# Kernel tuning notes

Hardware: AMD Instinct MI355X
Metric: run time of the kernel (lower is better)

The kernel has to match this reference:

```python
import math
import jax, jax.numpy as jnp
import numpy as np

B, S, D, H = 2, 2048, 1024, 16
HD = D // H  # head_dim = 64
LN_EPS = 1e-5


def setup_inputs() -> dict:
    key = jax.random.key(0)
    ks = jax.random.split(key, 12)
    scale = 1.0 / math.sqrt(D)
    inp = {
        "x": jax.random.normal(ks[0], (B, S, D), dtype=jnp.float32),
        "cdr_mask": jax.random.uniform(ks[1], (B, 1, S, S), dtype=jnp.float32),
        "Wq": jax.random.normal(ks[2], (D, D), dtype=jnp.float32) * scale,
        "bq": jnp.zeros((D,), dtype=jnp.float32),
        "Wk": jax.random.normal(ks[3], (D, D), dtype=jnp.float32) * scale,
        "bk": jnp.zeros((D,), dtype=jnp.float32),
        "Wv": jax.random.normal(ks[4], (D, D), dtype=jnp.float32) * scale,
        "bv": jnp.zeros((D,), dtype=jnp.float32),
        "Wo": jax.random.normal(ks[5], (D, D), dtype=jnp.float32) * scale,
        "bo": jnp.zeros((D,), dtype=jnp.float32),
        "gamma": jnp.ones((D,), dtype=jnp.float32),
        "beta": jnp.zeros((D,), dtype=jnp.float32),
        "cdr_weight": jnp.float32(1.0),
    }
    return inp


def _rotate_half(t):
    # even / odd interleaved halves, as in the torch module
    t1 = t[..., ::2]
    t2 = t[..., 1::2]
    return jnp.stack((-t2, t1), axis=-1).reshape(t.shape)


def reference(x, cdr_mask, Wq, bq, Wk, bk, Wv, bv, Wo, bo, gamma, beta, cdr_weight):
    b, s, d = x.shape
    # RoPE tables (concatenated, NOT interleaved -- faithful to source)
    inv_freq = 1.0 / (10000.0 ** (jnp.arange(0, HD, 2, dtype=jnp.float32) / HD))
    pos = jnp.arange(s, dtype=jnp.float32)
    sinusoid = pos[:, None] * inv_freq[None, :]          # [S, HD/2]
    sin_pos = jnp.concatenate([jnp.sin(sinusoid)] * 2, axis=-1)[None, None]  # [1,1,S,HD]
    cos_pos = jnp.concatenate([jnp.cos(sinusoid)] * 2, axis=-1)[None, None]

    def proj(W, bias):
        return (x @ W.T + bias).reshape(b, s, H, HD).transpose(0, 2, 1, 3)  # [B,H,S,HD]

    Q = proj(Wq, bq)
    K = proj(Wk, bk)
    V = proj(Wv, bv)
    Q = Q * cos_pos + _rotate_half(Q) * sin_pos
    K = K * cos_pos + _rotate_half(K) * sin_pos

    scores = jnp.einsum('bhqd,bhkd->bhqk', Q, K) / math.sqrt(HD)
    scores = scores + cdr_mask * cdr_weight
    probs = jax.nn.softmax(scores, axis=-1)
    attn = jnp.einsum('bhqk,bhkd->bhqd', probs, V)       # [B,H,S,HD]
    attn = attn.transpose(0, 2, 1, 3).reshape(b, s, d)
    out = attn @ Wo.T + bo                               # dropout is identity at eval

    y = x + out
    mu = jnp.mean(y, axis=-1, keepdims=True)
    var = jnp.var(y, axis=-1, keepdims=True)
    return (y - mu) / jnp.sqrt(var + LN_EPS) * gamma + beta
```

## Files before the change

kernel.cpp:

```cpp
#include <hip/hip_runtime.h>
#include <hip/hip_bf16.h>
#include <math.h>

#define Bn  2
#define Sn  2048
#define Dn  1024
#define Hn  16
#define HDn 64

typedef __attribute__((ext_vector_type(8))) short bf16x8;
typedef __attribute__((ext_vector_type(4))) short bf16x4;
typedef __attribute__((ext_vector_type(4))) float f32x4;

__device__ __forceinline__ uint2 pack4bf(float a, float b, float c, float d) {
    union { __hip_bfloat16 h[4]; uint2 u; } p;
    p.h[0] = __float2bfloat16(a); p.h[1] = __float2bfloat16(b);
    p.h[2] = __float2bfloat16(c); p.h[3] = __float2bfloat16(d);
    return p.u;
}

__device__ __forceinline__ bf16x4 pack4bfv(float a, float b, float c, float d) {
    union { __hip_bfloat16 h[4]; bf16x4 v; } p;
    p.h[0] = __float2bfloat16(a); p.h[1] = __float2bfloat16(b);
    p.h[2] = __float2bfloat16(c); p.h[3] = __float2bfloat16(d);
    return p.v;
}

__device__ __forceinline__ void g2l16(const __hip_bfloat16* g, __hip_bfloat16* lbase) {
    __builtin_amdgcn_global_load_lds(
        (const __attribute__((address_space(1))) void*)g,
        (__attribute__((address_space(3))) void*)lbase, 16, 0, 0);
}

__global__ __launch_bounds__(256) void cast_kernel(
    const float* __restrict__ in, __hip_bfloat16* __restrict__ out)
{
    const size_t i = ((size_t)blockIdx.x * 256 + threadIdx.x) * 4;
    float4 v = *(const float4*)(in + i);
    *(uint2*)(out + i) = pack4bf(v.x, v.y, v.z, v.w);
}

__global__ __launch_bounds__(256) void maskprep_kernel(
    const float* __restrict__ mask, const float* __restrict__ cwp,
    __hip_bfloat16* __restrict__ Mw)
{
    const int idx = blockIdx.x * 256 + threadIdx.x;
    const float cw = cwp[0];
    float4 v = ((const float4*)mask)[idx];
    ((uint2*)Mw)[idx] = pack4bf(v.x * cw, v.y * cw, v.z * cw, v.w * cw);
}

template<int MODE>
__global__ __launch_bounds__(256) void projmm(
    const __hip_bfloat16* __restrict__ X,
    const __hip_bfloat16* __restrict__ Wb,
    const float* __restrict__ bias,
    const float* __restrict__ resid,
    void* __restrict__ outp)
{
    __shared__ __hip_bfloat16 Xs[128 * 32];
    __shared__ __hip_bfloat16 Ws[64 * 32];
    const int tid  = threadIdx.x;
    const int w    = tid >> 6, lane = tid & 63;
    const int lrow = lane & 15, lhi = lane >> 4;
    const int m0   = blockIdx.y * 128, n0 = blockIdx.x * 64;
    const int rin  = lane >> 2, cbs = lane & 3;

    f32x4 acc[8];
#pragma unroll
    for (int i = 0; i < 8; i++) acc[i] = (f32x4){0.f, 0.f, 0.f, 0.f};

    for (int k0 = 0; k0 < Dn; k0 += 32) {
        const int xr0 = w * 32 + rin;
        const int xr1 = xr0 + 16;
        const int wr  = w * 16 + rin;
        g2l16(X  + (size_t)(m0 + xr0) * Dn + k0 + ((cbs ^ ((xr0 >> 1) & 3)) << 3),
              &Xs[(w * 32) * 32]);
        g2l16(X  + (size_t)(m0 + xr1) * Dn + k0 + ((cbs ^ ((xr1 >> 1) & 3)) << 3),
              &Xs[(w * 32 + 16) * 32]);
        g2l16(Wb + (size_t)(n0 + wr) * Dn + k0 + ((cbs ^ ((wr >> 1) & 3)) << 3),
              &Ws[(w * 16) * 32]);
        __syncthreads();

        bf16x8 FX[2], FW[4];
#pragma unroll
        for (int tm = 0; tm < 2; tm++) {
            const int r = w * 32 + tm * 16 + lrow;
            FX[tm] = *(const bf16x8*)&Xs[r * 32 + ((lhi ^ ((r >> 1) & 3)) << 3)];
        }
#pragma unroll
        for (int tn = 0; tn < 4; tn++) {
            const int r = tn * 16 + lrow;
            FW[tn] = *(const bf16x8*)&Ws[r * 32 + ((lhi ^ ((r >> 1) & 3)) << 3)];
        }
        if constexpr (MODE == 3) {
#pragma unroll
            for (int tm = 0; tm < 2; tm++)
#pragma unroll
                for (int tn = 0; tn < 4; tn++)
                    acc[tm * 4 + tn] = __builtin_amdgcn_mfma_f32_16x16x32_bf16(
                        FX[tm], FW[tn], acc[tm * 4 + tn], 0, 0, 0);
        } else {
#pragma unroll
            for (int tn = 0; tn < 4; tn++)
#pragma unroll
                for (int tm = 0; tm < 2; tm++)
                    acc[tn * 2 + tm] = __builtin_amdgcn_mfma_f32_16x16x32_bf16(
                        FW[tn], FX[tm], acc[tn * 2 + tm], 0, 0, 0);
        }
        __syncthreads();
    }

    const int h = n0 >> 6;

    if constexpr (MODE == 1 || MODE == 4) {
        __hip_bfloat16* outb = (__hip_bfloat16*)outp;
        const float NEG_L2C = -0.41524101186092033f;
#pragma unroll
        for (int tn = 0; tn < 4; tn++) {
            const int hd0 = tn * 16 + lhi * 4;
            const float4 b4 = *(const float4*)&bias[n0 + hd0];
            const float f0 = exp2f((float)((hd0 + 0) & 31) * NEG_L2C);
            const float f1 = exp2f((float)((hd0 + 1) & 31) * NEG_L2C);
            const float f2 = exp2f((float)((hd0 + 2) & 31) * NEG_L2C);
            const float f3 = exp2f((float)((hd0 + 3) & 31) * NEG_L2C);
#pragma unroll
            for (int tm = 0; tm < 2; tm++) {
                const int m = m0 + w * 32 + tm * 16 + lrow;
                const int s = m & (Sn - 1), bb = m >> 11;
                f32x4 a = acc[tn * 2 + tm];
                float v0 = a[0] + b4.x, v1 = a[1] + b4.y;
                float v2 = a[2] + b4.z, v3 = a[3] + b4.w;
                if (MODE == 1) { v0 *= 0.125f; v1 *= 0.125f; v2 *= 0.125f; v3 *= 0.125f; }
                const float sf = (float)s;
                const float c0 = __cosf(sf * f0), c1 = __cosf(sf * f1);
                const float c2 = __cosf(sf * f2), c3 = __cosf(sf * f3);
                const float s0 = __sinf(sf * f0), s1 = __sinf(sf * f1);
                const float s2 = __sinf(sf * f2), s3 = __sinf(sf * f3);
                const float r0 = v0 * c0 - v1 * s0;
                const float r1 = v1 * c1 + v0 * s1;
                const float r2 = v2 * c2 - v3 * s2;
                const float r3 = v3 * c3 + v2 * s3;
                *(uint2*)(outb + ((size_t)(bb * Hn + h) * Sn + s) * HDn + hd0) =
                    pack4bf(r0, r1, r2, r3);
            }
        }
    } else if constexpr (MODE == 3) {
        __hip_bfloat16* outb = (__hip_bfloat16*)outp;
#pragma unroll
        for (int tn = 0; tn < 4; tn++) {
            const int c = tn * 16 + lrow;
            const float bc = bias[n0 + c];
#pragma unroll
            for (int tm = 0; tm < 2; tm++) {
                const int mb = m0 + w * 32 + tm * 16 + lhi * 4;
                const int s = mb & (Sn - 1), bb = mb >> 11;
                f32x4 a = acc[tm * 4 + tn];
                *(uint2*)(outb + ((size_t)(bb * Hn + h) * HDn + c) * Sn + s) =
                    pack4bf(a[0] + bc, a[1] + bc, a[2] + bc, a[3] + bc);
            }
        }
    } else {
        float* outf = (float*)outp;
#pragma unroll
        for (int tn = 0; tn < 4; tn++) {
            const int nb = n0 + tn * 16 + lhi * 4;
            const float4 b4 = *(const float4*)&bias[nb];
#pragma unroll
            for (int tm = 0; tm < 2; tm++) {
                const int m = m0 + w * 32 + tm * 16 + lrow;
                f32x4 a = acc[tn * 2 + tm];
                const float4 rr = *(const float4*)&resid[(size_t)m * Dn + nb];
                *(float4*)(outf + (size_t)m * Dn + nb) =
                    make_float4(a[0] + b4.x + rr.x, a[1] + b4.y + rr.y,
                                a[2] + b4.z + rr.z, a[3] + b4.w + rr.w);
            }
        }
    }
}

struct __align__(16) TileBuf {
    __hip_bfloat16 K[64 * 64];
    __hip_bfloat16 V[64 * 64];
    __hip_bfloat16 M[64 * 64];
};

__device__ __forceinline__ void stage_tiles(
    TileBuf& t,
    const __hip_bfloat16* __restrict__ Kb,
    const __hip_bfloat16* __restrict__ Vb,
    const __hip_bfloat16* __restrict__ Mq0,
    int k0, int w, int lane)
{
#pragma unroll
    for (int j = 0; j < 2; j++) {
        const int row = w * 16 + j * 8 + (lane >> 3);
        const int blk = (lane & 7) ^ (row & 7);
        __hip_bfloat16* base = (__hip_bfloat16*)0;
        base = &((TileBuf&)t).K[(w * 16 + j * 8) * 64];
        g2l16(Kb + (size_t)(k0 + row) * HDn + blk * 8, base);
        base = &((TileBuf&)t).V[(w * 16 + j * 8) * 64];
        g2l16(Vb + (size_t)row * Sn + k0 + blk * 8, base);
        base = &((TileBuf&)t).M[(w * 16 + j * 8) * 64];
        g2l16(Mq0 + (size_t)row * Sn + k0 + blk * 8, base);
    }
}

__global__ __launch_bounds__(256) void attn_kernel(
    const __hip_bfloat16* __restrict__ Q,
    const __hip_bfloat16* __restrict__ K,
    const __hip_bfloat16* __restrict__ Vt,
    const __hip_bfloat16* __restrict__ Mw,
    __hip_bfloat16* __restrict__ A)
{
    __shared__ TileBuf tb[2];
    const int tid  = threadIdx.x;
    const int w    = tid >> 6, lane = tid & 63;
    const int lrow = lane & 15, lhi = lane >> 4;
    const int bh   = blockIdx.y, b = bh >> 4, h = bh & 15;
    const int q0   = blockIdx.x * 64;
    const int q    = q0 + w * 16 + lrow;

    const __hip_bfloat16* Qp  = Q + ((size_t)bh * Sn + q) * HDn + lhi * 8;
    const bf16x8 Qf0 = *(const bf16x8*)(Qp);
    const bf16x8 Qf1 = *(const bf16x8*)(Qp + 32);
    const __hip_bfloat16* Kb  = K  + (size_t)bh * Sn * HDn;
    const __hip_bfloat16* Vb  = Vt + (size_t)bh * HDn * Sn;
    const __hip_bfloat16* Mq0 = Mw + ((size_t)b * Sn + q0) * Sn;

    f32x4 Oc[4];
#pragma unroll
    for (int i = 0; i < 4; i++) Oc[i] = (f32x4){0.f, 0.f, 0.f, 0.f};
    float lsum = 0.f;

    stage_tiles(tb[0], Kb, Vb, Mq0, 0, w, lane);
    __syncthreads();

    for (int it = 0; it < Sn / 64; it++) {
        const int k0 = it * 64;
        if (it + 1 < Sn / 64)
            stage_tiles(tb[(it + 1) & 1], Kb, Vb, Mq0, k0 + 64, w, lane);
        const TileBuf& t = tb[it & 1];

        f32x4 st[4];
#pragma unroll
        for (int kt = 0; kt < 4; kt++) {
            const int rl = kt * 16 + lrow;
            const bf16x8 ka = *(const bf16x8*)&t.K[rl * 64 + ((lhi       ^ (rl & 7)) * 8)];
            const bf16x8 kc = *(const bf16x8*)&t.K[rl * 64 + (((4 + lhi) ^ (rl & 7)) * 8)];
            f32x4 z = (f32x4){0.f, 0.f, 0.f, 0.f};
            z = __builtin_amdgcn_mfma_f32_16x16x32_bf16(ka, Qf0, z, 0, 0, 0);
            z = __builtin_amdgcn_mfma_f32_16x16x32_bf16(kc, Qf1, z, 0, 0, 0);
            st[kt] = z;
        }

        const int rq = w * 16 + lrow;
        bf16x4 pk[4];
#pragma unroll
        for (int kt = 0; kt < 4; kt++) {
            const int eo = (((2 * kt + (lhi >> 1)) ^ (rq & 7)) * 8) + (lhi & 1) * 4;
            union { uint2 u; __hip_bfloat16 hh[4]; } mu;
            mu.u = *(const uint2*)&t.M[rq * 64 + eo];
            const float p0 = __expf(st[kt][0] + __bfloat162float(mu.hh[0]));
            const float p1 = __expf(st[kt][1] + __bfloat162float(mu.hh[1]));
            const float p2 = __expf(st[kt][2] + __bfloat162float(mu.hh[2]));
            const float p3 = __expf(st[kt][3] + __bfloat162float(mu.hh[3]));
            lsum += (p0 + p1) + (p2 + p3);
            pk[kt] = pack4bfv(p0, p1, p2, p3);
        }

#pragma unroll
        for (int ch = 0; ch < 4; ch++) {
            const int rv = ch * 16 + lrow;
#pragma unroll
            for (int kt = 0; kt < 4; kt++) {
                const int eo = (((2 * kt + (lhi >> 1)) ^ (rv & 7)) * 8) + (lhi & 1) * 4;
                const bf16x4 vf = *(const bf16x4*)&t.V[rv * 64 + eo];
                Oc[ch] = __builtin_amdgcn_mfma_f32_16x16x16bf16_1k(
                    vf, pk[kt], Oc[ch], 0, 0, 0);
            }
        }
        __syncthreads();
    }

    lsum += __shfl_xor(lsum, 16, 64);
    lsum += __shfl_xor(lsum, 32, 64);
    const float inv = 1.f / lsum;

    __hip_bfloat16* ap = A + ((size_t)(b * Sn + q)) * Dn + h * HDn;
#pragma unroll
    for (int ch = 0; ch < 4; ch++) {
        *(uint2*)(ap + ch * 16 + lhi * 4) =
            pack4bf(Oc[ch][0] * inv, Oc[ch][1] * inv, Oc[ch][2] * inv, Oc[ch][3] * inv);
    }
}

__global__ __launch_bounds__(256) void ln_kernel(
    const float* __restrict__ Yin, const float* __restrict__ gamma,
    const float* __restrict__ beta, float* __restrict__ out)
{
    __shared__ float red[256];
    const int m   = blockIdx.x;
    const int tid = threadIdx.x;
    const size_t base = (size_t)m * Dn + tid * 4;
    float4 y = *(const float4*)(Yin + base);

    red[tid] = y.x + y.y + y.z + y.w; __syncthreads();
    for (int off = 128; off > 0; off >>= 1) {
        if (tid < off) red[tid] += red[tid + off];
        __syncthreads();
    }
    const float mu = red[0] * (1.f / Dn);
    __syncthreads();

    const float d0 = y.x - mu, d1 = y.y - mu, d2 = y.z - mu, d3 = y.w - mu;
    red[tid] = d0*d0 + d1*d1 + d2*d2 + d3*d3; __syncthreads();
    for (int off = 128; off > 0; off >>= 1) {
        if (tid < off) red[tid] += red[tid + off];
        __syncthreads();
    }
    const float var = red[0] * (1.f / Dn);
    const float rin = rsqrtf(var + 1e-5f);

    float4 gv = *(const float4*)(gamma + tid * 4);
    float4 bv = *(const float4*)(beta  + tid * 4);
    *(float4*)(out + base) = make_float4(d0 * rin * gv.x + bv.x,
                                         d1 * rin * gv.y + bv.y,
                                         d2 * rin * gv.z + bv.z,
                                         d3 * rin * gv.w + bv.w);
}

extern "C" void kernel_launch(void* const* d_in, const int* in_sizes, int n_in,
                              void* d_out, int out_size, void* d_ws, size_t ws_size,
                              hipStream_t stream)
{
    const float* x     = (const float*)d_in[0];
    const float* mask  = (const float*)d_in[1];
    const float* Wq    = (const float*)d_in[2];
    const float* bq    = (const float*)d_in[3];
    const float* Wk    = (const float*)d_in[4];
    const float* bk    = (const float*)d_in[5];
    const float* Wv    = (const float*)d_in[6];
    const float* bv    = (const float*)d_in[7];
    const float* Wo    = (const float*)d_in[8];
    const float* bo    = (const float*)d_in[9];
    const float* gamma = (const float*)d_in[10];
    const float* beta  = (const float*)d_in[11];
    const float* cw    = (const float*)d_in[12];
    float* out = (float*)d_out;

    const size_t MB = 1024 * 1024;
    char* ws = (char*)d_ws;
    __hip_bfloat16* Xb  = (__hip_bfloat16*)(ws);
    __hip_bfloat16* Qb  = (__hip_bfloat16*)(ws +  8 * MB);
    __hip_bfloat16* Kb  = (__hip_bfloat16*)(ws + 16 * MB);
    __hip_bfloat16* Vtb = (__hip_bfloat16*)(ws + 24 * MB);
    __hip_bfloat16* Mw  = (__hip_bfloat16*)(ws + 32 * MB);
    __hip_bfloat16* Wqb = (__hip_bfloat16*)(ws + 48 * MB);
    __hip_bfloat16* Wkb = (__hip_bfloat16*)(ws + 50 * MB);
    __hip_bfloat16* Wvb = (__hip_bfloat16*)(ws + 52 * MB);
    __hip_bfloat16* Wob = (__hip_bfloat16*)(ws + 54 * MB);
    __hip_bfloat16* Ab  = Xb;

    cast_kernel<<<4096, 256, 0, stream>>>(x,  Xb);
    cast_kernel<<<1024, 256, 0, stream>>>(Wq, Wqb);
    cast_kernel<<<1024, 256, 0, stream>>>(Wk, Wkb);
    cast_kernel<<<1024, 256, 0, stream>>>(Wv, Wvb);
    cast_kernel<<<1024, 256, 0, stream>>>(Wo, Wob);
    maskprep_kernel<<<(Bn * Sn * Sn / 4) / 256, 256, 0, stream>>>(mask, cw, Mw);

    dim3 g(Dn / 64, (Bn * Sn) / 128);
    projmm<1><<<g, 256, 0, stream>>>(Xb, Wqb, bq, nullptr, Qb);
    projmm<4><<<g, 256, 0, stream>>>(Xb, Wkb, bk, nullptr, Kb);
    projmm<3><<<g, 256, 0, stream>>>(Xb, Wvb, bv, nullptr, Vtb);
    attn_kernel<<<dim3(Sn / 64, Bn * Hn), 256, 0, stream>>>(Qb, Kb, Vtb, Mw, Ab);
    projmm<2><<<g, 256, 0, stream>>>(Ab, Wob, bo, x, out);
    ln_kernel<<<Bn * Sn, 256, 0, stream>>>(out, gamma, beta, out);
}
```

Baseline: 304.2 us.

## Enlarge projection GEMM tiles, use exp2 softmax, warp-shuffle LayerNorm, paired bf16 packing

Projection GEMMs move from 128x64 to 128x128 block tiles with a 2x2 wave layout, so each wave computes a 64x64 subtile and more work is reused per LDS load. The grid halves, which may reduce occupancy. The softmax pre-scales Q and the mask by log2(e) so attention can use the hardware exp2 instead of __expf. LayerNorm replaces the shared-memory tree reductions with wave shuffles and a single-pass sum and sum-of-squares, which is slightly less numerically stable. bf16 packing now uses paired conversions.

```diff
diff --git a/kernel.cpp b/kernel.cpp
--- a/kernel.cpp
+++ b/kernel.cpp
@@ -12,17 +12,23 @@
 typedef __attribute__((ext_vector_type(4))) short bf16x4;
 typedef __attribute__((ext_vector_type(4))) float f32x4;
 
+#define LOG2E 1.44269504088896340736f
+
+__device__ __forceinline__ float fexp2(float x) {
+    return __builtin_amdgcn_exp2f(x);
+}
+
 __device__ __forceinline__ uint2 pack4bf(float a, float b, float c, float d) {
-    union { __hip_bfloat16 h[4]; uint2 u; } p;
-    p.h[0] = __float2bfloat16(a); p.h[1] = __float2bfloat16(b);
-    p.h[2] = __float2bfloat16(c); p.h[3] = __float2bfloat16(d);
+    union { __hip_bfloat162 h2[2]; uint2 u; } p;
+    p.h2[0] = __float22bfloat162_rn(make_float2(a, b));
+    p.h2[1] = __float22bfloat162_rn(make_float2(c, d));
     return p.u;
 }
 
 __device__ __forceinline__ bf16x4 pack4bfv(float a, float b, float c, float d) {
-    union { __hip_bfloat16 h[4]; bf16x4 v; } p;
-    p.h[0] = __float2bfloat16(a); p.h[1] = __float2bfloat16(b);
-    p.h[2] = __float2bfloat16(c); p.h[3] = __float2bfloat16(d);
+    union { __hip_bfloat162 h2[2]; bf16x4 v; } p;
+    p.h2[0] = __float22bfloat162_rn(make_float2(a, b));
+    p.h2[1] = __float22bfloat162_rn(make_float2(c, d));
     return p.v;
 }
 
@@ -45,7 +51,7 @@
     __hip_bfloat16* __restrict__ Mw)
 {
     const int idx = blockIdx.x * 256 + threadIdx.x;
-    const float cw = cwp[0];
+    const float cw = cwp[0] * LOG2E;
     float4 v = ((const float4*)mask)[idx];
     ((uint2*)Mw)[idx] = pack4bf(v.x * cw, v.y * cw, v.z * cw, v.w * cw);
 }
@@ -59,43 +65,40 @@
     void* __restrict__ outp)
 {
     __shared__ __hip_bfloat16 Xs[128 * 32];
-    __shared__ __hip_bfloat16 Ws[64 * 32];
+    __shared__ __hip_bfloat16 Ws[128 * 32];
     const int tid  = threadIdx.x;
     const int w    = tid >> 6, lane = tid & 63;
     const int lrow = lane & 15, lhi = lane >> 4;
-    const int m0   = blockIdx.y * 128, n0 = blockIdx.x * 64;
-    const int rin  = lane >> 2, cbs = lane & 3;
-
-    f32x4 acc[8];
-#pragma unroll
-    for (int i = 0; i < 8; i++) acc[i] = (f32x4){0.f, 0.f, 0.f, 0.f};
+    const int m0   = blockIdx.y * 128, n0 = blockIdx.x * 128;
+    const int rm   = (w & 1) * 64;
+    const int rn   = (w >> 1) * 64;
+    const int srow = lane >> 2, cb = lane & 3;
+
+    f32x4 acc[16];
+#pragma unroll
+    for (int i = 0; i < 16; i++) acc[i] = (f32x4){0.f, 0.f, 0.f, 0.f};
 
     for (int k0 = 0; k0 < Dn; k0 += 32) {
-        const int xr0 = w * 32 + rin;
-        const int xr1 = xr0 + 16;
-        const int wr  = w * 16 + rin;
-        g2l16(X  + (size_t)(m0 + xr0) * Dn + k0 + ((cbs ^ ((xr0 >> 1) & 3)) << 3),
-              &Xs[(w * 32) * 32]);
-        g2l16(X  + (size_t)(m0 + xr1) * Dn + k0 + ((cbs ^ ((xr1 >> 1) & 3)) << 3),
-              &Xs[(w * 32 + 16) * 32]);
-        g2l16(Wb + (size_t)(n0 + wr) * Dn + k0 + ((cbs ^ ((wr >> 1) & 3)) << 3),
-              &Ws[(w * 16) * 32]);
+#pragma unroll
+        for (int j = 0; j < 2; j++) {
+            const int row = w * 32 + j * 16 + srow;
+            const int sc  = (cb ^ ((row >> 1) & 3)) << 3;
+            g2l16(X  + (size_t)(m0 + row) * Dn + k0 + sc, &Xs[(w * 32 + j * 16) * 32]);
+            g2l16(Wb + (size_t)(n0 + row) * Dn + k0 + sc, &Ws[(w * 32 + j * 16) * 32]);
+        }
         __syncthreads();
 
-        bf16x8 FX[2], FW[4];
-#pragma unroll
-        for (int tm = 0; tm < 2; tm++) {
-            const int r = w * 32 + tm * 16 + lrow;
-            FX[tm] = *(const bf16x8*)&Xs[r * 32 + ((lhi ^ ((r >> 1) & 3)) << 3)];
-        }
-#pragma unroll
-        for (int tn = 0; tn < 4; tn++) {
-            const int r = tn * 16 + lrow;
-            FW[tn] = *(const bf16x8*)&Ws[r * 32 + ((lhi ^ ((r >> 1) & 3)) << 3)];
+        bf16x8 FX[4], FW[4];
+#pragma unroll
+        for (int t = 0; t < 4; t++) {
+            const int ra = rm + t * 16 + lrow;
+            FX[t] = *(const bf16x8*)&Xs[ra * 32 + ((lhi ^ ((ra >> 1) & 3)) << 3)];
+            const int rb = rn + t * 16 + lrow;
+            FW[t] = *(const bf16x8*)&Ws[rb * 32 + ((lhi ^ ((rb >> 1) & 3)) << 3)];
         }
         if constexpr (MODE == 3) {
 #pragma unroll
-            for (int tm = 0; tm < 2; tm++)
+            for (int tm = 0; tm < 4; tm++)
 #pragma unroll
                 for (int tn = 0; tn < 4; tn++)
                     acc[tm * 4 + tn] = __builtin_amdgcn_mfma_f32_16x16x32_bf16(
@@ -104,34 +107,34 @@
 #pragma unroll
             for (int tn = 0; tn < 4; tn++)
 #pragma unroll
-                for (int tm = 0; tm < 2; tm++)
-                    acc[tn * 2 + tm] = __builtin_amdgcn_mfma_f32_16x16x32_bf16(
-                        FW[tn], FX[tm], acc[tn * 2 + tm], 0, 0, 0);
+                for (int tm = 0; tm < 4; tm++)
+                    acc[tn * 4 + tm] = __builtin_amdgcn_mfma_f32_16x16x32_bf16(
+                        FW[tn], FX[tm], acc[tn * 4 + tm], 0, 0, 0);
         }
         __syncthreads();
     }
-
-    const int h = n0 >> 6;
 
     if constexpr (MODE == 1 || MODE == 4) {
         __hip_bfloat16* outb = (__hip_bfloat16*)outp;
+        const int h = (n0 >> 6) + (w >> 1);
         const float NEG_L2C = -0.41524101186092033f;
+        const float SCL = 0.125f * LOG2E;
 #pragma unroll
         for (int tn = 0; tn < 4; tn++) {
             const int hd0 = tn * 16 + lhi * 4;
-            const float4 b4 = *(const float4*)&bias[n0 + hd0];
+            const float4 b4 = *(const float4*)&bias[n0 + rn + hd0];
             const float f0 = exp2f((float)((hd0 + 0) & 31) * NEG_L2C);
             const float f1 = exp2f((float)((hd0 + 1) & 31) * NEG_L2C);
             const float f2 = exp2f((float)((hd0 + 2) & 31) * NEG_L2C);
             const float f3 = exp2f((float)((hd0 + 3) & 31) * NEG_L2C);
 #pragma unroll
-            for (int tm = 0; tm < 2; tm++) {
-                const int m = m0 + w * 32 + tm * 16 + lrow;
+            for (int tm = 0; tm < 4; tm++) {
+                const int m = m0 + rm + tm * 16 + lrow;
                 const int s = m & (Sn - 1), bb = m >> 11;
-                f32x4 a = acc[tn * 2 + tm];
+                f32x4 a = acc[tn * 4 + tm];
                 float v0 = a[0] + b4.x, v1 = a[1] + b4.y;
                 float v2 = a[2] + b4.z, v3 = a[3] + b4.w;
-                if (MODE == 1) { v0 *= 0.125f; v1 *= 0.125f; v2 *= 0.125f; v3 *= 0.125f; }
+                if (MODE == 1) { v0 *= SCL; v1 *= SCL; v2 *= SCL; v3 *= SCL; }
                 const float sf = (float)s;
                 const float c0 = __cosf(sf * f0), c1 = __cosf(sf * f1);
                 const float c2 = __cosf(sf * f2), c3 = __cosf(sf * f3);
@@ -147,13 +150,14 @@
         }
     } else if constexpr (MODE == 3) {
         __hip_bfloat16* outb = (__hip_bfloat16*)outp;
+        const int h = (n0 >> 6) + (w >> 1);
 #pragma unroll
         for (int tn = 0; tn < 4; tn++) {
             const int c = tn * 16 + lrow;
-            const float bc = bias[n0 + c];
-#pragma unroll
-            for (int tm = 0; tm < 2; tm++) {
-                const int mb = m0 + w * 32 + tm * 16 + lhi * 4;
+            const float bc = bias[n0 + rn + c];
+#pragma unroll
+            for (int tm = 0; tm < 4; tm++) {
+                const int mb = m0 + rm + tm * 16 + lhi * 4;
                 const int s = mb & (Sn - 1), bb = mb >> 11;
                 f32x4 a = acc[tm * 4 + tn];
                 *(uint2*)(outb + ((size_t)(bb * Hn + h) * HDn + c) * Sn + s) =
@@ -164,12 +168,12 @@
         float* outf = (float*)outp;
 #pragma unroll
         for (int tn = 0; tn < 4; tn++) {
-            const int nb = n0 + tn * 16 + lhi * 4;
+            const int nb = n0 + rn + tn * 16 + lhi * 4;
             const float4 b4 = *(const float4*)&bias[nb];
 #pragma unroll
-            for (int tm = 0; tm < 2; tm++) {
-                const int m = m0 + w * 32 + tm * 16 + lrow;
-                f32x4 a = acc[tn * 2 + tm];
+            for (int tm = 0; tm < 4; tm++) {
+                const int m = m0 + rm + tm * 16 + lrow;
+                f32x4 a = acc[tn * 4 + tm];
                 const float4 rr = *(const float4*)&resid[(size_t)m * Dn + nb];
                 *(float4*)(outf + (size_t)m * Dn + nb) =
                     make_float4(a[0] + b4.x + rr.x, a[1] + b4.y + rr.y,
@@ -196,13 +200,9 @@
     for (int j = 0; j < 2; j++) {
         const int row = w * 16 + j * 8 + (lane >> 3);
         const int blk = (lane & 7) ^ (row & 7);
-        __hip_bfloat16* base = (__hip_bfloat16*)0;
-        base = &((TileBuf&)t).K[(w * 16 + j * 8) * 64];
-        g2l16(Kb + (size_t)(k0 + row) * HDn + blk * 8, base);
-        base = &((TileBuf&)t).V[(w * 16 + j * 8) * 64];
-        g2l16(Vb + (size_t)row * Sn + k0 + blk * 8, base);
-        base = &((TileBuf&)t).M[(w * 16 + j * 8) * 64];
-        g2l16(Mq0 + (size_t)row * Sn + k0 + blk * 8, base);
+        g2l16(Kb + (size_t)(k0 + row) * HDn + blk * 8, &t.K[(w * 16 + j * 8) * 64]);
+        g2l16(Vb + (size_t)row * Sn + k0 + blk * 8,    &t.V[(w * 16 + j * 8) * 64]);
+        g2l16(Mq0 + (size_t)row * Sn + k0 + blk * 8,   &t.M[(w * 16 + j * 8) * 64]);
     }
 }
 
@@ -261,10 +261,10 @@
             const int eo = (((2 * kt + (lhi >> 1)) ^ (rq & 7)) * 8) + (lhi & 1) * 4;
             union { uint2 u; __hip_bfloat16 hh[4]; } mu;
             mu.u = *(const uint2*)&t.M[rq * 64 + eo];
-            const float p0 = __expf(st[kt][0] + __bfloat162float(mu.hh[0]));
-            const float p1 = __expf(st[kt][1] + __bfloat162float(mu.hh[1]));
-            const float p2 = __expf(st[kt][2] + __bfloat162float(mu.hh[2]));
-            const float p3 = __expf(st[kt][3] + __bfloat162float(mu.hh[3]));
+            const float p0 = fexp2(st[kt][0] + __bfloat162float(mu.hh[0]));
+            const float p1 = fexp2(st[kt][1] + __bfloat162float(mu.hh[1]));
+            const float p2 = fexp2(st[kt][2] + __bfloat162float(mu.hh[2]));
+            const float p3 = fexp2(st[kt][3] + __bfloat162float(mu.hh[3]));
             lsum += (p0 + p1) + (p2 + p3);
             pk[kt] = pack4bfv(p0, p1, p2, p3);
         }
@@ -299,35 +299,33 @@
     const float* __restrict__ Yin, const float* __restrict__ gamma,
     const float* __restrict__ beta, float* __restrict__ out)
 {
-    __shared__ float red[256];
+    __shared__ float2 wred[4];
     const int m   = blockIdx.x;
     const int tid = threadIdx.x;
     const size_t base = (size_t)m * Dn + tid * 4;
     float4 y = *(const float4*)(Yin + base);
 
-    red[tid] = y.x + y.y + y.z + y.w; __syncthreads();
-    for (int off = 128; off > 0; off >>= 1) {
-        if (tid < off) red[tid] += red[tid + off];
-        __syncthreads();
-    }
-    const float mu = red[0] * (1.f / Dn);
+    float s1 = y.x + y.y + y.z + y.w;
+    float s2 = y.x * y.x + y.y * y.y + y.z * y.z + y.w * y.w;
+#pragma unroll
+    for (int off = 32; off; off >>= 1) {
+        s1 += __shfl_xor(s1, off, 64);
+        s2 += __shfl_xor(s2, off, 64);
+    }
+    if ((tid & 63) == 0) wred[tid >> 6] = make_float2(s1, s2);
     __syncthreads();
-
-    const float d0 = y.x - mu, d1 = y.y - mu, d2 = y.z - mu, d3 = y.w - mu;
-    red[tid] = d0*d0 + d1*d1 + d2*d2 + d3*d3; __syncthreads();
-    for (int off = 128; off > 0; off >>= 1) {
-        if (tid < off) red[tid] += red[tid + off];
-        __syncthreads();
-    }
-    const float var = red[0] * (1.f / Dn);
+    const float S1 = wred[0].x + wred[1].x + wred[2].x + wred[3].x;
+    const float S2 = wred[0].y + wred[1].y + wred[2].y + wred[3].y;
+    const float mu  = S1 * (1.f / Dn);
+    const float var = S2 * (1.f / Dn) - mu * mu;
     const float rin = rsqrtf(var + 1e-5f);
 
     float4 gv = *(const float4*)(gamma + tid * 4);
     float4 bv = *(const float4*)(beta  + tid * 4);
-    *(float4*)(out + base) = make_float4(d0 * rin * gv.x + bv.x,
-                                         d1 * rin * gv.y + bv.y,
-                                         d2 * rin * gv.z + bv.z,
-                                         d3 * rin * gv.w + bv.w);
+    *(float4*)(out + base) = make_float4((y.x - mu) * rin * gv.x + bv.x,
+                                         (y.y - mu) * rin * gv.y + bv.y,
+                                         (y.z - mu) * rin * gv.z + bv.z,
+                                         (y.w - mu) * rin * gv.w + bv.w);
 }
 
 extern "C" void kernel_launch(void* const* d_in, const int* in_sizes, int n_in,
@@ -369,7 +367,7 @@
     cast_kernel<<<1024, 256, 0, stream>>>(Wo, Wob);
     maskprep_kernel<<<(Bn * Sn * Sn / 4) / 256, 256, 0, stream>>>(mask, cw, Mw);
 
-    dim3 g(Dn / 64, (Bn * Sn) / 128);
+    dim3 g(Dn / 128, (Bn * Sn) / 128);
     projmm<1><<<g, 256, 0, stream>>>(Xb, Wqb, bq, nullptr, Qb);
     projmm<4><<<g, 256, 0, stream>>>(Xb, Wkb, bk, nullptr, Kb);
     projmm<3><<<g, 256, 0, stream>>>(Xb, Wvb, bv, nullptr, Vtb);
```

Result: no change. 306.5 us (+0.8%).
